# Performance work log

Hardware: AMD Instinct MI355X
Metric: run time of the kernel (lower is better)

Reference implementation:

```python
import jax, jax.numpy as jnp
import numpy as np
import math

G, NPG, D = 64, 2048, 128   # graphs, nodes per graph, feature dim
DEG = 16
N = G * NPG
E = N * DEG
VOCAB = 100000
RATIO = 0.8


def setup_inputs() -> dict:
    key = jax.random.key(0)
    ks = jax.random.split(key, 24)
    node_ids = jax.random.randint(ks[0], (N, 1), 0, VOCAB)
    # within-graph edges: endpoints in [0, NPG) per graph, then add graph offset
    within = jax.random.randint(ks[1], (2, G, NPG * DEG), 0, NPG)
    offs = (jnp.arange(G) * NPG)[None, :, None]
    edge_index = (within + offs).reshape(2, E)
    batch = jnp.repeat(jnp.arange(G), NPG)
    f = lambda k, shape: jax.random.normal(k, shape, dtype=jnp.float32) * 0.05
    return dict(
        node_ids=node_ids, edge_index=edge_index, batch=batch,
        emb=f(ks[2], (VOCAB, D)),
        Wl1=f(ks[3], (D, D)), Wr1=f(ks[4], (D, D)), bl1=f(ks[5], (D,)), pw1=f(ks[6], (D,)),
        Wl2=f(ks[7], (D, D)), Wr2=f(ks[8], (D, D)), bl2=f(ks[9], (D,)), pw2=f(ks[10], (D,)),
        Wl3=f(ks[11], (D, D)), Wr3=f(ks[12], (D, D)), bl3=f(ks[13], (D,)), pw3=f(ks[14], (D,)),
        W1=f(ks[15], (128, 256)), b1=f(ks[16], (128,)),
        W2=f(ks[17], (64, 128)), b2=f(ks[18], (64,)),
        W3=f(ks[19], (1, 64)), b3=f(ks[20], (1,)),
    )


def sage(x, src, dst, emask, Wl, bl, Wr):
    # PyG SAGEConv (mean aggr): lin_l(mean_j x_j) + lin_r(x_i); lin_r has no bias
    n = x.shape[0]
    msg = x[src] * emask[:, None].astype(x.dtype)
    dstm = jnp.where(emask, dst, n)  # dummy segment for invalid edges
    s = jax.ops.segment_sum(msg, dstm, num_segments=n + 1)[:n]
    c = jax.ops.segment_sum(emask.astype(x.dtype), dstm, num_segments=n + 1)[:n]
    mean = s / jnp.maximum(c, 1.0)[:, None]
    return mean @ Wl.T + bl + x @ Wr.T


def topk_pool(x, src, dst, emask, w, n_per):
    # PyG TopKPooling: score = tanh(x.w/||w||), keep top ceil(ratio*n) per graph,
    # scale kept features by score, remap/filter edges.
    n = x.shape[0]
    g = n // n_per
    k = math.ceil(RATIO * n_per)
    score = jnp.tanh((x @ w) / jnp.linalg.norm(w))
    ts, ti = jax.lax.top_k(score.reshape(g, n_per), k)  # [g, k]
    perm = (ti + (jnp.arange(g) * n_per)[:, None]).reshape(-1)  # old global idx
    x_new = x[perm] * ts.reshape(-1)[:, None]
    n_new = g * k
    new_of_old = jnp.full((n,), n_new, dtype=jnp.int32).at[perm].set(
        jnp.arange(n_new, dtype=jnp.int32))
    sn, dn = new_of_old[src], new_of_old[dst]
    em = emask & (sn < n_new) & (dn < n_new)
    sn = jnp.where(em, sn, 0)
    dn = jnp.where(em, dn, n_new)
    return x_new, sn, dn, em, k


def readout(x, k):
    # cat([global_max_pool, global_mean_pool]) with equal-size graphs
    g = x.shape[0] // k
    xr = x.reshape(g, k, -1)
    return jnp.concatenate([xr.max(axis=1), xr.mean(axis=1)], axis=1)


def reference(node_ids, edge_index, batch, emb,
              Wl1, Wr1, bl1, pw1, Wl2, Wr2, bl2, pw2, Wl3, Wr3, bl3, pw3,
              W1, b1, W2, b2, W3, b3):
    x = emb[node_ids.squeeze(1)]                       # [N, 128]
    src, dst = edge_index[0], edge_index[1]
    em = jnp.ones((src.shape[0],), dtype=bool)

    x = jax.nn.relu(sage(x, src, dst, em, Wl1, bl1, Wr1))
    x, src, dst, em, k1 = topk_pool(x, src, dst, em, pw1, NPG)
    x1 = readout(x, k1)

    x = jax.nn.relu(sage(x, src, dst, em, Wl2, bl2, Wr2))
    x, src, dst, em, k2 = topk_pool(x, src, dst, em, pw2, k1)
    x2 = readout(x, k2)

    x = jax.nn.relu(sage(x, src, dst, em, Wl3, bl3, Wr3))
    x, src, dst, em, k3 = topk_pool(x, src, dst, em, pw3, k2)
    x3 = readout(x, k3)

    h = x1 + x2 + x3                                   # [G, 256]
    h = jax.nn.relu(h @ W1.T + b1)
    h = jax.nn.relu(h @ W2.T + b2)                     # dropout = identity (eval)
    return jax.nn.sigmoid(h @ W3.T + b3).squeeze(1)    # [G]
```

## Files before the change

kernel.cpp:

```cpp
#include <hip/hip_runtime.h>
#include <hip/hip_bf16.h>
#include <float.h>

typedef _Float16 f16x8 __attribute__((ext_vector_type(8)));
typedef float f32x4 __attribute__((ext_vector_type(4)));

#define GRAPHS 64
#define NPG 2048
#define DIM 128
#define NNODES (GRAPHS * NPG)
#define NEDGES (NNODES * 16)
#define ECAP 32768
#define NSB 8
#define RSLICES 16
#define RPB 256

__global__ __launch_bounds__(256) void embed_kernel(const int* __restrict__ ids,
    const float* __restrict__ emb, _Float16* __restrict__ xh) {
  int idx = blockIdx.x * 256 + threadIdx.x;
  int nd = idx >> 4, part = idx & 15;
  int id = ids[nd];
  const float* src = emb + (size_t)id * 128 + part * 8;
  float4 a = *(const float4*)(src);
  float4 b = *(const float4*)(src + 4);
  f16x8 o;
  o[0] = (_Float16)a.x; o[1] = (_Float16)a.y; o[2] = (_Float16)a.z; o[3] = (_Float16)a.w;
  o[4] = (_Float16)b.x; o[5] = (_Float16)b.y; o[6] = (_Float16)b.z; o[7] = (_Float16)b.w;
  *(f16x8*)(xh + (size_t)nd * 128 + part * 8) = o;
}

__global__ __launch_bounds__(256) void convert_w(const float* __restrict__ Wl,
    const float* __restrict__ Wr, _Float16* __restrict__ wh) {
  int qq = blockIdx.x * 256 + threadIdx.x;
  int ks = qq >> 9, nf = (qq >> 6) & 7, l = qq & 63;
  int ncol = nf * 16 + (l & 15);
  int k0 = (ks & 3) * 32 + ((l >> 4) << 3);
  const float* wsrc = ((ks < 4) ? Wl : Wr) + ncol * 128 + k0;
  float4 a = *(const float4*)wsrc;
  float4 b = *(const float4*)(wsrc + 4);
  f16x8 w;
  w[0] = (_Float16)a.x; w[1] = (_Float16)a.y; w[2] = (_Float16)a.z; w[3] = (_Float16)a.w;
  w[4] = (_Float16)b.x; w[5] = (_Float16)b.y; w[6] = (_Float16)b.z; w[7] = (_Float16)b.w;
  *(f16x8*)(wh + (size_t)qq * 8) = w;
}

__global__ __launch_bounds__(1024) void csr_hist(const int* __restrict__ src,
    const int* __restrict__ dst, int np, int* __restrict__ part) {
  __shared__ int hist[2048];
  int x = blockIdx.x;
  int s = x & 7, q = x >> 3;
  int b = q & (NSB - 1), gh = q >> 3;
  int g = gh * 8 + s;
  int tid = threadIdx.x;
  for (int i = tid; i < 2048; i += 1024) hist[i] = 0;
  __syncthreads();
  int e0 = g * ECAP + b * (ECAP / NSB);
  int nodebase = g * np;
  for (int e = tid; e < ECAP / NSB; e += 1024) {
    atomicAdd(&hist[dst[e0 + e] - nodebase], 1);
  }
  __syncthreads();
  for (int i = tid; i < np; i += 1024) part[((size_t)(g * NSB + b)) * 2048 + i] = hist[i];
}

__global__ __launch_bounds__(1024) void csr_scan(const int* __restrict__ part, int np,
    int* __restrict__ offb, int* __restrict__ deg, int* __restrict__ curs) {
  __shared__ int psum[1024];
  int g = blockIdx.x, tid = threadIdx.x;
  int i0 = 2 * tid, i1 = 2 * tid + 1;
  int p0[NSB], p1[NSB];
  int c0 = 0, c1 = 0;
#pragma unroll
  for (int b = 0; b < NSB; ++b) {
    p0[b] = (i0 < np) ? part[((size_t)(g * NSB + b)) * 2048 + i0] : 0;
    p1[b] = (i1 < np) ? part[((size_t)(g * NSB + b)) * 2048 + i1] : 0;
    c0 += p0[b]; c1 += p1[b];
  }
  int pair = c0 + c1;
  psum[tid] = pair;
  for (int s = 1; s < 1024; s <<= 1) {
    __syncthreads();
    int t = (tid >= s) ? psum[tid - s] : 0;
    __syncthreads();
    psum[tid] += t;
  }
  int excl = psum[tid] - pair;
  int ebase = g * ECAP;
  int nodebase = g * np;
  if (i0 < np) {
    int off = ebase + excl;
    offb[nodebase + i0] = off;
    deg[nodebase + i0] = c0;
    int cur = off;
#pragma unroll
    for (int b = 0; b < NSB; ++b) { curs[((size_t)(g * NSB + b)) * 2048 + i0] = cur; cur += p0[b]; }
  }
  if (i1 < np) {
    int off = ebase + excl + c0;
    offb[nodebase + i1] = off;
    deg[nodebase + i1] = c1;
    int cur = off;
#pragma unroll
    for (int b = 0; b < NSB; ++b) { curs[((size_t)(g * NSB + b)) * 2048 + i1] = cur; cur += p1[b]; }
  }
}

__global__ __launch_bounds__(1024) void csr_place(const int* __restrict__ src,
    const int* __restrict__ dst, int np, const int* __restrict__ curs,
    int* __restrict__ esort) {
  __shared__ int cur[2048];
  int x = blockIdx.x;
  int s = x & 7, q = x >> 3;
  int b = q & (NSB - 1), gh = q >> 3;
  int g = gh * 8 + s;
  int tid = threadIdx.x;
  for (int i = tid; i < np; i += 1024) cur[i] = curs[((size_t)(g * NSB + b)) * 2048 + i];
  __syncthreads();
  int e0 = g * ECAP + b * (ECAP / NSB);
  int nodebase = g * np;
  for (int e = tid; e < ECAP / NSB; e += 1024) {
    int ge = e0 + e;
    int p = atomicAdd(&cur[dst[ge] - nodebase], 1);
    esort[p] = src[ge];
  }
}

__global__ __launch_bounds__(256) void compose_kernel(int* __restrict__ A,
    const int* __restrict__ B, int n) {
  int v = blockIdx.x * 256 + threadIdx.x;
  if (v >= n) return;
  int a = A[v];
  A[v] = (a >= 0) ? B[a] : -1;
}

__global__ __launch_bounds__(256) void remap_esort(const int* __restrict__ esort0,
    const int* __restrict__ noo, int* __restrict__ esortl, int E4) {
  int t = blockIdx.x * 256 + threadIdx.x;
  if (t >= E4) return;
  int4 s = *(const int4*)(esort0 + t * 4);
  int4 o;
  o.x = noo[s.x]; o.y = noo[s.y]; o.z = noo[s.z]; o.w = noo[s.w];
  *(int4*)(esortl + t * 4) = o;
}

__global__ __launch_bounds__(256) void aggregate_kernel(const _Float16* __restrict__ xh,
    const int* __restrict__ offb, const int* __restrict__ deg, const int* __restrict__ esrc,
    _Float16* __restrict__ meanh, int np, int C) {
  int bid = blockIdx.x;
  int s = bid & 7, q = bid >> 3;
  int gsub = q / C, chunk = q - gsub * C;
  int g = gsub * 8 + s;
  int wave = threadIdx.x >> 6, lane = threadIdx.x & 63;
  int sub = lane >> 4, l = lane & 15;
  int local = chunk * 16 + wave * 4 + sub;
  if (local >= np) return;
  int w = g * np + local;
  int b = offb[w], c = deg[w];
  int e = b + c;
  float acc[8] = {0.f, 0.f, 0.f, 0.f, 0.f, 0.f, 0.f, 0.f};
  int i = b;
  for (; i + 4 <= e; i += 4) {
    int s0 = esrc[i], s1 = esrc[i + 1], s2 = esrc[i + 2], s3 = esrc[i + 3];
    f16x8 v0 = *(const f16x8*)(xh + (size_t)s0 * 128 + l * 8);
    f16x8 v1 = *(const f16x8*)(xh + (size_t)s1 * 128 + l * 8);
    f16x8 v2 = *(const f16x8*)(xh + (size_t)s2 * 128 + l * 8);
    f16x8 v3 = *(const f16x8*)(xh + (size_t)s3 * 128 + l * 8);
    f16x8 t = (v0 + v1) + (v2 + v3);
#pragma unroll
    for (int j = 0; j < 8; ++j) acc[j] += (float)t[j];
  }
  for (; i < e; ++i) {
    int srcn = esrc[i];
    f16x8 v = *(const f16x8*)(xh + (size_t)srcn * 128 + l * 8);
#pragma unroll
    for (int j = 0; j < 8; ++j) acc[j] += (float)v[j];
  }
  float inv = 1.f / (float)(c > 0 ? c : 1);
  f16x8 o;
#pragma unroll
  for (int j = 0; j < 8; ++j) o[j] = (_Float16)(acc[j] * inv);
  *(f16x8*)(meanh + (size_t)w * 128 + l * 8) = o;
}

__global__ __launch_bounds__(256) void aggregate_f(const _Float16* __restrict__ xh,
    const int* __restrict__ offb0, const int* __restrict__ deg0, const int* __restrict__ esortl,
    const int* __restrict__ orig, _Float16* __restrict__ meanh, int np, int C) {
  int bid = blockIdx.x;
  int s = bid & 7, q = bid >> 3;
  int gsub = q / C, chunk = q - gsub * C;
  int g = gsub * 8 + s;
  int wave = threadIdx.x >> 6, lane = threadIdx.x & 63;
  int sub = lane >> 4, l = lane & 15;
  int local = chunk * 16 + wave * 4 + sub;
  if (local >= np) return;
  int w = g * np + local;
  int o = orig[w];
  int b = offb0[o], c0 = deg0[o];
  int e = b + c0;
  float acc[8] = {0.f, 0.f, 0.f, 0.f, 0.f, 0.f, 0.f, 0.f};
  int cnt = 0;
  const f16x8 zero = {(_Float16)0.f, (_Float16)0.f, (_Float16)0.f, (_Float16)0.f,
                      (_Float16)0.f, (_Float16)0.f, (_Float16)0.f, (_Float16)0.f};
  int i = b;
  for (; i + 4 <= e; i += 4) {
    int n0 = esortl[i], n1 = esortl[i + 1], n2 = esortl[i + 2], n3 = esortl[i + 3];
    f16x8 v0 = zero, v1 = zero, v2 = zero, v3 = zero;
    if (n0 >= 0) v0 = *(const f16x8*)(xh + (size_t)n0 * 128 + l * 8);
    if (n1 >= 0) v1 = *(const f16x8*)(xh + (size_t)n1 * 128 + l * 8);
    if (n2 >= 0) v2 = *(const f16x8*)(xh + (size_t)n2 * 128 + l * 8);
    if (n3 >= 0) v3 = *(const f16x8*)(xh + (size_t)n3 * 128 + l * 8);
    cnt += (n0 >= 0) + (n1 >= 0) + (n2 >= 0) + (n3 >= 0);
    f16x8 t = (v0 + v1) + (v2 + v3);
#pragma unroll
    for (int j = 0; j < 8; ++j) acc[j] += (float)t[j];
  }
  for (; i < e; ++i) {
    int sn = esortl[i];
    if (sn < 0) continue;
    ++cnt;
    f16x8 v = *(const f16x8*)(xh + (size_t)sn * 128 + l * 8);
#pragma unroll
    for (int j = 0; j < 8; ++j) acc[j] += (float)v[j];
  }
  float inv = 1.f / (float)(cnt > 0 ? cnt : 1);
  f16x8 ov;
#pragma unroll
  for (int j = 0; j < 8; ++j) ov[j] = (_Float16)(acc[j] * inv);
  *(f16x8*)(meanh + (size_t)w * 128 + l * 8) = ov;
}

__global__ __launch_bounds__(256, 2) void sage_gemm(const _Float16* __restrict__ XH,
    const _Float16* MEANIN, _Float16* OUT, const _Float16* __restrict__ WH,
    const float* __restrict__ bl, const float* __restrict__ pw, float* __restrict__ sc,
    int n) {
  __shared__ _Float16 WB[4096 * 8];
  int tid = threadIdx.x;
  for (int qq = tid; qq < 4096; qq += 256)
    *(f16x8*)(WB + qq * 8) = *(const f16x8*)(WH + (size_t)qq * 8);
  __syncthreads();
  int wave = tid >> 6, lane = tid & 63;
  int wrow0 = blockIdx.x * RPB + wave * 64;
  if (wrow0 >= n) return;
  int kb = (lane >> 4) << 3;
  int lr = lane & 15;
  f32x4 acc[4][8];
#pragma unroll
  for (int t = 0; t < 4; ++t)
#pragma unroll
    for (int nf = 0; nf < 8; ++nf) acc[t][nf] = (f32x4){0.f, 0.f, 0.f, 0.f};
#pragma unroll
  for (int ks = 0; ks < 8; ++ks) {
    const _Float16* A = (ks < 4) ? MEANIN : XH;
    const _Float16* ap = A + (size_t)(wrow0 + lr) * 128 + (ks & 3) * 32 + kb;
    f16x8 a0 = *(const f16x8*)(ap);
    f16x8 a1 = *(const f16x8*)(ap + 16 * 128);
    f16x8 a2 = *(const f16x8*)(ap + 32 * 128);
    f16x8 a3 = *(const f16x8*)(ap + 48 * 128);
#pragma unroll
    for (int nf = 0; nf < 8; ++nf) {
      f16x8 b = *(const f16x8*)(WB + ((ks * 8 + nf) * 64 + lane) * 8);
      acc[0][nf] = __builtin_amdgcn_mfma_f32_16x16x32_f16(a0, b, acc[0][nf], 0, 0, 0);
      acc[1][nf] = __builtin_amdgcn_mfma_f32_16x16x32_f16(a1, b, acc[1][nf], 0, 0, 0);
      acc[2][nf] = __builtin_amdgcn_mfma_f32_16x16x32_f16(a2, b, acc[2][nf], 0, 0, 0);
      acc[3][nf] = __builtin_amdgcn_mfma_f32_16x16x32_f16(a3, b, acc[3][nf], 0, 0, 0);
    }
  }
  float pwv[8], qn = 0.f;
#pragma unroll
  for (int nf = 0; nf < 8; ++nf) {
    pwv[nf] = pw[nf * 16 + lr];
    qn += pwv[nf] * pwv[nf];
  }
#pragma unroll
  for (int o = 1; o < 16; o <<= 1) qn += __shfl_xor(qn, o);
  float inv_n = 1.f / sqrtf(qn);
#pragma unroll
  for (int t = 0; t < 4; ++t) {
    int rbase = wrow0 + t * 16 + ((lane >> 4) << 2);
    float dot[4] = {0.f, 0.f, 0.f, 0.f};
#pragma unroll
    for (int nf = 0; nf < 8; ++nf) {
      int col = nf * 16 + lr;
      float bias = bl[col];
#pragma unroll
      for (int r = 0; r < 4; ++r) {
        float v = fmaxf(acc[t][nf][r] + bias, 0.f);
        OUT[(size_t)(rbase + r) * 128 + col] = (_Float16)v;
        dot[r] += v * pwv[nf];
      }
    }
#pragma unroll
    for (int r = 0; r < 4; ++r) {
#pragma unroll
      for (int o = 1; o < 16; o <<= 1) dot[r] += __shfl_xor(dot[r], o);
    }
    if (lr == 0) {
#pragma unroll
      for (int r = 0; r < 4; ++r) sc[rbase + r] = tanhf(dot[r] * inv_n);
    }
  }
}

__global__ __launch_bounds__(1024) void topk_kernel(const float* __restrict__ sc, int n_per, int k,
    float* __restrict__ ts, int* __restrict__ perm, int* __restrict__ noo) {
  __shared__ unsigned long long L[2048];
  int g = blockIdx.x;
  int tid = threadIdx.x;
  int lane = tid & 63, wave = tid >> 6;
  int i0 = wave * 128 + lane;
  int i1 = i0 + 64;
  const float* scg = sc + g * n_per;
  auto keyize = [&](int i) -> unsigned long long {
    float f = (i < n_per) ? scg[i] : -FLT_MAX;
    unsigned u = __float_as_uint(f);
    u = (u & 0x80000000u) ? ~u : (u | 0x80000000u);
    return ((unsigned long long)u << 32) | (unsigned)(2047 - i);
  };
  unsigned long long a = keyize(i0), b = keyize(i1);
#pragma clang loop unroll(disable)
  for (unsigned kk = 2; kk <= 2048; kk <<= 1) {
#pragma clang loop unroll(disable)
    for (unsigned j = kk >> 1; j >= 128; j >>= 1) {
      L[i0] = a; L[i1] = b;
      __syncthreads();
      unsigned long long pa = L[i0 ^ j], pb = L[i1 ^ j];
      bool dA = ((i0 & kk) == 0), lA = ((i0 & j) == 0);
      if ((dA == lA) ? (pa > a) : (pa < a)) a = pa;
      bool dB = ((i1 & kk) == 0), lB = ((i1 & j) == 0);
      if ((dB == lB) ? (pb > b) : (pb < b)) b = pb;
      __syncthreads();
    }
    if (kk >= 128) {
      bool desc = ((i0 & kk) == 0);
      if ((a < b) == desc) { unsigned long long t = a; a = b; b = t; }
    }
    unsigned jtop = (kk >> 1 < 32u) ? (kk >> 1) : 32u;
#pragma clang loop unroll(disable)
    for (unsigned j = jtop; j >= 1; j >>= 1) {
      unsigned long long oa = __shfl_xor(a, (int)j);
      unsigned long long ob = __shfl_xor(b, (int)j);
      bool low = ((lane & j) == 0);
      bool dA = ((i0 & kk) == 0);
      if ((dA == low) ? (oa > a) : (oa < a)) a = oa;
      bool dB = ((i1 & kk) == 0);
      if ((dB == low) ? (ob > b) : (ob < b)) b = ob;
    }
  }
  auto emit = [&](unsigned long long v, int rank) {
    int orig = 2047 - (int)(v & 0xFFFFFFFFu);
    if (orig < n_per) {
      if (rank < k) {
        int ng = g * k + rank;
        ts[ng] = scg[orig];
        perm[ng] = g * n_per + orig;
        noo[g * n_per + orig] = ng;
      } else {
        noo[g * n_per + orig] = -1;
      }
    }
  };
  emit(a, i0);
  emit(b, i1);
}

__global__ __launch_bounds__(256) void gather_kernel(const _Float16* __restrict__ xold,
    const int* __restrict__ perm, const float* __restrict__ ts, _Float16* __restrict__ xh,
    const int* __restrict__ orig_in, int* __restrict__ orig_out, int n_new) {
  int idx = blockIdx.x * 256 + threadIdx.x;
  int v = idx >> 4, part = idx & 15;
  if (v >= n_new) return;
  int p = perm[v];
  if (part == 0) orig_out[v] = orig_in ? orig_in[p] : p;
  float t = ts[v];
  f16x8 a = *(const f16x8*)(xold + (size_t)p * 128 + part * 8);
  f16x8 o;
#pragma unroll
  for (int j = 0; j < 8; ++j) o[j] = (_Float16)((float)a[j] * t);
  *(f16x8*)(xh + (size_t)v * 128 + part * 8) = o;
}

__global__ __launch_bounds__(256) void readout_part(const _Float16* __restrict__ x, int k,
    float* __restrict__ pmax, float* __restrict__ psum) {
  int g = blockIdx.x >> 4;
  int slice = blockIdx.x & (RSLICES - 1);
  int d = threadIdx.x & 127;
  int half = threadIdx.x >> 7;
  int rpb = (k + RSLICES - 1) / RSLICES;
  int r0 = slice * rpb;
  int r1 = r0 + rpb; if (r1 > k) r1 = k;
  float vmax = -FLT_MAX, vs = 0.f;
  for (int r = r0 + half; r < r1; r += 2) {
    float v = (float)x[((size_t)g * k + r) * 128 + d];
    vmax = fmaxf(vmax, v);
    vs += v;
  }
  __shared__ float smax[256], ssum[256];
  smax[threadIdx.x] = vmax;
  ssum[threadIdx.x] = vs;
  __syncthreads();
  if (threadIdx.x < 128) {
    vmax = fmaxf(smax[threadIdx.x], smax[threadIdx.x + 128]);
    vs = ssum[threadIdx.x] + ssum[threadIdx.x + 128];
    pmax[(size_t)(g * RSLICES + slice) * 128 + d] = vmax;
    psum[(size_t)(g * RSLICES + slice) * 128 + d] = vs;
  }
}

__global__ __launch_bounds__(256) void readout_comb(const float* __restrict__ pmax,
    const float* __restrict__ psum, int k, float* __restrict__ h) {
  int idx = blockIdx.x * 256 + threadIdx.x;
  int g = idx >> 7, d = idx & 127;
  float vmax = -FLT_MAX, vs = 0.f;
#pragma unroll
  for (int s = 0; s < RSLICES; ++s) {
    vmax = fmaxf(vmax, pmax[(size_t)(g * RSLICES + s) * 128 + d]);
    vs += psum[(size_t)(g * RSLICES + s) * 128 + d];
  }
  h[g * 256 + d] += vmax;
  h[g * 256 + 128 + d] += vs / (float)k;
}

__global__ __launch_bounds__(256) void mlp1(const float* __restrict__ h, const float* __restrict__ W1,
    const float* __restrict__ b1, float* __restrict__ h1) {
  int o = blockIdx.x * 256 + threadIdx.x;
  int g = o >> 7, j = o & 127;
  const float* hp = h + g * 256;
  const float* wp = W1 + j * 256;
  float a = b1[j];
  for (int c = 0; c < 256; ++c) a += hp[c] * wp[c];
  h1[o] = fmaxf(a, 0.f);
}

__global__ __launch_bounds__(256) void mlp2(const float* __restrict__ h1, const float* __restrict__ W2,
    const float* __restrict__ b2, float* __restrict__ h2) {
  int o = blockIdx.x * 256 + threadIdx.x;
  int g = o >> 6, j = o & 63;
  const float* hp = h1 + g * 128;
  const float* wp = W2 + j * 128;
  float a = b2[j];
  for (int c = 0; c < 128; ++c) a += hp[c] * wp[c];
  h2[o] = fmaxf(a, 0.f);
}

__global__ __launch_bounds__(64) void mlp3(const float* __restrict__ h2, const float* __restrict__ W3,
    const float* __restrict__ b3, float* __restrict__ out) {
  int g = threadIdx.x;
  if (g >= 64) return;
  const float* hp = h2 + g * 64;
  float a = b3[0];
  for (int c = 0; c < 64; ++c) a += hp[c] * W3[c];
  out[g] = 1.f / (1.f + expf(-a));
}

extern "C" void kernel_launch(void* const* d_in, const int* in_sizes, int n_in,
                              void* d_out, int out_size, void* d_ws, size_t ws_size,
                              hipStream_t stream) {
  const int* node_ids = (const int*)d_in[0];
  const int* ei = (const int*)d_in[1];
  const float* emb = (const float*)d_in[3];
  const float* W[3][4] = {
      {(const float*)d_in[4], (const float*)d_in[5], (const float*)d_in[6], (const float*)d_in[7]},
      {(const float*)d_in[8], (const float*)d_in[9], (const float*)d_in[10], (const float*)d_in[11]},
      {(const float*)d_in[12], (const float*)d_in[13], (const float*)d_in[14], (const float*)d_in[15]}};
  const float* W1 = (const float*)d_in[16];
  const float* b1 = (const float*)d_in[17];
  const float* W2 = (const float*)d_in[18];
  const float* b2 = (const float*)d_in[19];
  const float* W3 = (const float*)d_in[20];
  const float* b3 = (const float*)d_in[21];
  float* out = (float*)d_out;

  const int E = NEDGES;
  char* ws = (char*)d_ws;
  size_t o = 0;
  auto alloc = [&](size_t bytes) { void* p = ws + o; o = (o + bytes + 255) & ~(size_t)255; return p; };
  _Float16* XH = (_Float16*)alloc((size_t)NNODES * 128 * 2);
  _Float16* MEANH = (_Float16*)alloc((size_t)NNODES * 128 * 2);
  int* ESORT = (int*)alloc((size_t)E * 4);
  int* ESORTL = (int*)alloc((size_t)E * 4);
  int* PART = (int*)alloc((size_t)GRAPHS * NSB * 2048 * 4);
  int* CURS = (int*)alloc((size_t)GRAPHS * NSB * 2048 * 4);
  int* OFFB = (int*)alloc((size_t)NNODES * 4);
  int* DEG = (int*)alloc((size_t)NNODES * 4);
  float* SC = (float*)alloc((size_t)NNODES * 4);
  float* TS = (float*)alloc((size_t)NNODES * 4);
  int* PERM = (int*)alloc((size_t)NNODES * 4);
  int* NOOA = (int*)alloc((size_t)NNODES * 4);
  int* NOOB = (int*)alloc((size_t)NNODES * 4);
  int* ORIGA = (int*)alloc((size_t)NNODES * 4);
  int* ORIGB = (int*)alloc((size_t)NNODES * 4);
  _Float16* WH0 = (_Float16*)alloc(4096 * 8 * 2);
  _Float16* WH1 = (_Float16*)alloc(4096 * 8 * 2);
  _Float16* WH2 = (_Float16*)alloc(4096 * 8 * 2);
  float* PMAX = (float*)alloc((size_t)GRAPHS * RSLICES * 128 * 4);
  float* PSUM = (float*)alloc((size_t)GRAPHS * RSLICES * 128 * 4);
  float* H = (float*)alloc(64 * 256 * 4);
  float* H1 = (float*)alloc(64 * 128 * 4);
  float* H2 = (float*)alloc(64 * 64 * 4);

  embed_kernel<<<NNODES * 16 / 256, 256, 0, stream>>>(node_ids, emb, XH);
  hipMemsetAsync(H, 0, 64 * 256 * 4, stream);
  convert_w<<<16, 256, 0, stream>>>(W[0][0], W[0][1], WH0);
  convert_w<<<16, 256, 0, stream>>>(W[1][0], W[1][1], WH1);
  convert_w<<<16, 256, 0, stream>>>(W[2][0], W[2][1], WH2);

  const int* src = ei;
  const int* dst = ei + E;
  csr_hist<<<GRAPHS * NSB, 1024, 0, stream>>>(src, dst, NPG, PART);
  csr_scan<<<GRAPHS, 1024, 0, stream>>>(PART, NPG, OFFB, DEG, CURS);
  csr_place<<<GRAPHS * NSB, 1024, 0, stream>>>(src, dst, NPG, CURS, ESORT);

  struct LayerP { int n, k; };
  LayerP L[3] = {{131072, 1639}, {104896, 1312}, {83968, 1050}};
  _Float16* WHs[3] = {WH0, WH1, WH2};
  int* ORIG_cur = ORIGA;
  int* ORIG_next = ORIGB;

  for (int li = 0; li < 3; ++li) {
    int n = L[li].n, k = L[li].k;
    int np = n / 64;
    int n_new = 64 * k;
    const float *bl = W[li][2], *pw = W[li][3];

    int C = (np + 15) / 16;
    if (li == 0) {
      aggregate_kernel<<<64 * C, 256, 0, stream>>>(XH, OFFB, DEG, ESORT, MEANH, np, C);
    } else {
      remap_esort<<<E / 4 / 256, 256, 0, stream>>>(ESORT, NOOA, ESORTL, E / 4);
      aggregate_f<<<64 * C, 256, 0, stream>>>(XH, OFFB, DEG, ESORTL, ORIG_cur,
                                              MEANH, np, C);
    }
    sage_gemm<<<(n + RPB - 1) / RPB, 256, 0, stream>>>(XH, MEANH, MEANH, WHs[li], bl, pw, SC, n);
    topk_kernel<<<GRAPHS, 1024, 0, stream>>>(SC, np, k, TS, PERM, (li == 0) ? NOOA : NOOB);
    gather_kernel<<<n_new * 16 / 256, 256, 0, stream>>>(MEANH, PERM, TS, XH,
        (li == 0) ? nullptr : ORIG_cur, ORIG_next, n_new);
    { int* t = ORIG_cur; ORIG_cur = ORIG_next; ORIG_next = t; }
    readout_part<<<GRAPHS * RSLICES, 256, 0, stream>>>(XH, k, PMAX, PSUM);
    readout_comb<<<32, 256, 0, stream>>>(PMAX, PSUM, k, H);
    if (li == 1) compose_kernel<<<NNODES / 256, 256, 0, stream>>>(NOOA, NOOB, NNODES);
  }

  mlp1<<<32, 256, 0, stream>>>(H, W1, b1, H1);
  mlp2<<<16, 256, 0, stream>>>(H1, W2, b2, H2);
  mlp3<<<1, 64, 0, stream>>>(H2, W3, b3, out);
}
```

Before: 393.3 us.

## Fuse top-k selection, gather, readout and index composition into one kernel

Merges topk, gather, readout_part/readout_comb and compose_kernel into a single per-graph kernel. The sorted keys stay in shared memory and drive the gather directly, the max/mean readout is accumulated while gathering, and the old-to-new index map is composed in shared memory instead of in a separate global pass. This removes four launches per layer and the round trips through global memory for the PERM, TS, PMAX and PSUM buffers. The cost is that only 64 blocks (one per graph) now do the gather and readout, which lowers parallelism for that memory-bound work.

Result: faster. 367.7 us (-6.5%).

```diff
diff --git a/kernel.cpp b/kernel.cpp
--- a/kernel.cpp
+++ b/kernel.cpp
@@ -12,7 +12,6 @@
 #define NEDGES (NNODES * 16)
 #define ECAP 32768
 #define NSB 8
-#define RSLICES 16
 #define RPB 256
 
 __global__ __launch_bounds__(256) void embed_kernel(const int* __restrict__ ids,
@@ -123,14 +122,6 @@
     int p = atomicAdd(&cur[dst[ge] - nodebase], 1);
     esort[p] = src[ge];
   }
-}
-
-__global__ __launch_bounds__(256) void compose_kernel(int* __restrict__ A,
-    const int* __restrict__ B, int n) {
-  int v = blockIdx.x * 256 + threadIdx.x;
-  if (v >= n) return;
-  int a = A[v];
-  A[v] = (a >= 0) ? B[a] : -1;
 }
 
 __global__ __launch_bounds__(256) void remap_esort(const int* __restrict__ esort0,
@@ -301,9 +292,14 @@
   }
 }
 
-__global__ __launch_bounds__(1024) void topk_kernel(const float* __restrict__ sc, int n_per, int k,
-    float* __restrict__ ts, int* __restrict__ perm, int* __restrict__ noo) {
+__global__ __launch_bounds__(1024) void topk_fused(const float* __restrict__ sc,
+    int n_per, int k, const _Float16* __restrict__ meanin, _Float16* __restrict__ xh,
+    int* __restrict__ nooA, const int* __restrict__ orig_in, int* __restrict__ orig_out,
+    float* __restrict__ h, int mode) {
   __shared__ unsigned long long L[2048];
+  __shared__ int c2n[2048];
+  __shared__ float redmax[2048];
+  __shared__ float redsum[2048];
   int g = blockIdx.x;
   int tid = threadIdx.x;
   int lane = tid & 63, wave = tid >> 6;
@@ -346,78 +342,69 @@
       if ((dB == low) ? (ob > b) : (ob < b)) b = ob;
     }
   }
-  auto emit = [&](unsigned long long v, int rank) {
-    int orig = 2047 - (int)(v & 0xFFFFFFFFu);
-    if (orig < n_per) {
-      if (rank < k) {
-        int ng = g * k + rank;
-        ts[ng] = scg[orig];
-        perm[ng] = g * n_per + orig;
-        noo[g * n_per + orig] = ng;
-      } else {
-        noo[g * n_per + orig] = -1;
-      }
-    }
-  };
-  emit(a, i0);
-  emit(b, i1);
-}
-
-__global__ __launch_bounds__(256) void gather_kernel(const _Float16* __restrict__ xold,
-    const int* __restrict__ perm, const float* __restrict__ ts, _Float16* __restrict__ xh,
-    const int* __restrict__ orig_in, int* __restrict__ orig_out, int n_new) {
-  int idx = blockIdx.x * 256 + threadIdx.x;
-  int v = idx >> 4, part = idx & 15;
-  if (v >= n_new) return;
-  int p = perm[v];
-  if (part == 0) orig_out[v] = orig_in ? orig_in[p] : p;
-  float t = ts[v];
-  f16x8 a = *(const f16x8*)(xold + (size_t)p * 128 + part * 8);
-  f16x8 o;
-#pragma unroll
-  for (int j = 0; j < 8; ++j) o[j] = (_Float16)((float)a[j] * t);
-  *(f16x8*)(xh + (size_t)v * 128 + part * 8) = o;
-}
-
-__global__ __launch_bounds__(256) void readout_part(const _Float16* __restrict__ x, int k,
-    float* __restrict__ pmax, float* __restrict__ psum) {
-  int g = blockIdx.x >> 4;
-  int slice = blockIdx.x & (RSLICES - 1);
-  int d = threadIdx.x & 127;
-  int half = threadIdx.x >> 7;
-  int rpb = (k + RSLICES - 1) / RSLICES;
-  int r0 = slice * rpb;
-  int r1 = r0 + rpb; if (r1 > k) r1 = k;
-  float vmax = -FLT_MAX, vs = 0.f;
-  for (int r = r0 + half; r < r1; r += 2) {
-    float v = (float)x[((size_t)g * k + r) * 128 + d];
-    vmax = fmaxf(vmax, v);
-    vs += v;
-  }
-  __shared__ float smax[256], ssum[256];
-  smax[threadIdx.x] = vmax;
-  ssum[threadIdx.x] = vs;
+  L[i0] = a; L[i1] = b;
+  int orig_a = 2047 - (int)(a & 0xFFFFFFFFu);
+  int orig_b = 2047 - (int)(b & 0xFFFFFFFFu);
+  if (mode == 0) {
+    if (orig_a < n_per) nooA[g * n_per + orig_a] = (i0 < k) ? g * k + i0 : -1;
+    if (orig_b < n_per) nooA[g * n_per + orig_b] = (i1 < k) ? g * k + i1 : -1;
+  } else if (mode == 1) {
+    if (orig_a < n_per) c2n[orig_a] = (i0 < k) ? g * k + i0 : -1;
+    if (orig_b < n_per) c2n[orig_b] = (i1 < k) ? g * k + i1 : -1;
+  }
   __syncthreads();
-  if (threadIdx.x < 128) {
-    vmax = fmaxf(smax[threadIdx.x], smax[threadIdx.x + 128]);
-    vs = ssum[threadIdx.x] + ssum[threadIdx.x + 128];
-    pmax[(size_t)(g * RSLICES + slice) * 128 + d] = vmax;
-    psum[(size_t)(g * RSLICES + slice) * 128 + d] = vs;
-  }
-}
-
-__global__ __launch_bounds__(256) void readout_comb(const float* __restrict__ pmax,
-    const float* __restrict__ psum, int k, float* __restrict__ h) {
-  int idx = blockIdx.x * 256 + threadIdx.x;
-  int g = idx >> 7, d = idx & 127;
-  float vmax = -FLT_MAX, vs = 0.f;
-#pragma unroll
-  for (int s = 0; s < RSLICES; ++s) {
-    vmax = fmaxf(vmax, pmax[(size_t)(g * RSLICES + s) * 128 + d]);
-    vs += psum[(size_t)(g * RSLICES + s) * 128 + d];
-  }
-  h[g * 256 + d] += vmax;
-  h[g * 256 + 128 + d] += vs / (float)k;
+  if (mode == 1) {
+    for (int o2 = tid; o2 < NPG; o2 += 1024) {
+      int a0 = nooA[g * NPG + o2];
+      nooA[g * NPG + o2] = (a0 >= 0) ? c2n[a0 - g * n_per] : -1;
+    }
+  }
+  int grp = tid >> 4, l8 = tid & 15;
+  float vmax[8], vsum[8];
+#pragma unroll
+  for (int j = 0; j < 8; ++j) { vmax[j] = -FLT_MAX; vsum[j] = 0.f; }
+  for (int r = grp; r < k; r += 64) {
+    unsigned long long key = L[r];
+    int orig = 2047 - (int)(key & 0xFFFFFFFFu);
+    int p = g * n_per + orig;
+    float score = scg[orig];
+    f16x8 v = *(const f16x8*)(meanin + (size_t)p * 128 + l8 * 8);
+    f16x8 ovv;
+#pragma unroll
+    for (int j = 0; j < 8; ++j) {
+      float val = (float)v[j] * score;
+      ovv[j] = (_Float16)val;
+      vmax[j] = fmaxf(vmax[j], val);
+      vsum[j] += val;
+    }
+    *(f16x8*)(xh + (size_t)(g * k + r) * 128 + l8 * 8) = ovv;
+    if (l8 == 0) orig_out[g * k + r] = orig_in ? orig_in[p] : p;
+  }
+#pragma unroll
+  for (int j = 0; j < 8; ++j) {
+    vmax[j] = fmaxf(vmax[j], __shfl_xor(vmax[j], 16));
+    vmax[j] = fmaxf(vmax[j], __shfl_xor(vmax[j], 32));
+    vsum[j] += __shfl_xor(vsum[j], 16);
+    vsum[j] += __shfl_xor(vsum[j], 32);
+  }
+  if ((lane >> 4) == 0) {
+#pragma unroll
+    for (int j = 0; j < 8; ++j) {
+      redmax[wave * 128 + l8 * 8 + j] = vmax[j];
+      redsum[wave * 128 + l8 * 8 + j] = vsum[j];
+    }
+  }
+  __syncthreads();
+  if (tid < 128) {
+    float m = -FLT_MAX, s2 = 0.f;
+#pragma unroll
+    for (int wv = 0; wv < 16; ++wv) {
+      m = fmaxf(m, redmax[wv * 128 + tid]);
+      s2 += redsum[wv * 128 + tid];
+    }
+    h[g * 256 + tid] += m;
+    h[g * 256 + 128 + tid] += s2 / (float)k;
+  }
 }
 
 __global__ __launch_bounds__(256) void mlp1(const float* __restrict__ h, const float* __restrict__ W1,
@@ -483,17 +470,12 @@
   int* OFFB = (int*)alloc((size_t)NNODES * 4);
   int* DEG = (int*)alloc((size_t)NNODES * 4);
   float* SC = (float*)alloc((size_t)NNODES * 4);
-  float* TS = (float*)alloc((size_t)NNODES * 4);
-  int* PERM = (int*)alloc((size_t)NNODES * 4);
   int* NOOA = (int*)alloc((size_t)NNODES * 4);
-  int* NOOB = (int*)alloc((size_t)NNODES * 4);
   int* ORIGA = (int*)alloc((size_t)NNODES * 4);
   int* ORIGB = (int*)alloc((size_t)NNODES * 4);
   _Float16* WH0 = (_Float16*)alloc(4096 * 8 * 2);
   _Float16* WH1 = (_Float16*)alloc(4096 * 8 * 2);
   _Float16* WH2 = (_Float16*)alloc(4096 * 8 * 2);
-  float* PMAX = (float*)alloc((size_t)GRAPHS * RSLICES * 128 * 4);
-  float* PSUM = (float*)alloc((size_t)GRAPHS * RSLICES * 128 * 4);
   float* H = (float*)alloc(64 * 256 * 4);
   float* H1 = (float*)alloc(64 * 128 * 4);
   float* H2 = (float*)alloc(64 * 64 * 4);
@@ -519,7 +501,6 @@
   for (int li = 0; li < 3; ++li) {
     int n = L[li].n, k = L[li].k;
     int np = n / 64;
-    int n_new = 64 * k;
     const float *bl = W[li][2], *pw = W[li][3];
 
     int C = (np + 15) / 16;
@@ -531,13 +512,9 @@
                                               MEANH, np, C);
     }
     sage_gemm<<<(n + RPB - 1) / RPB, 256, 0, stream>>>(XH, MEANH, MEANH, WHs[li], bl, pw, SC, n);
-    topk_kernel<<<GRAPHS, 1024, 0, stream>>>(SC, np, k, TS, PERM, (li == 0) ? NOOA : NOOB);
-    gather_kernel<<<n_new * 16 / 256, 256, 0, stream>>>(MEANH, PERM, TS, XH,
-        (li == 0) ? nullptr : ORIG_cur, ORIG_next, n_new);
+    topk_fused<<<GRAPHS, 1024, 0, stream>>>(SC, np, k, MEANH, XH, NOOA,
+        (li == 0) ? nullptr : ORIG_cur, ORIG_next, H, li);
     { int* t = ORIG_cur; ORIG_cur = ORIG_next; ORIG_next = t; }
-    readout_part<<<GRAPHS * RSLICES, 256, 0, stream>>>(XH, k, PMAX, PSUM);
-    readout_comb<<<32, 256, 0, stream>>>(PMAX, PSUM, k, H);
-    if (li == 1) compose_kernel<<<NNODES / 256, 256, 0, stream>>>(NOOA, NOOB, NNODES);
   }
 
   mlp1<<<32, 256, 0, stream>>>(H, W1, b1, H1);
```
